# Optimization experiments

Measured on AMD Instinct MI355X. Metric: run time of the kernel, lower is better.

The kernel has to match this reference:

```python
import jax, jax.numpy as jnp
import numpy as np

B, T, EEG, GEO, TH, HID, OUT = 4096, 320, 64, 18, 32, 16, 4
THETA0, BETA, TAU_A, TAU_M, EPS = 0.5, 1.8, 0.36, 0.8, 1e-5


@jax.custom_vjp
def spike_fn(x):
    return jnp.where(x >= 0, 1.0, 0.0).astype(x.dtype)

def _spike_fwd(x):
    return spike_fn(x), x

def _spike_bwd(x, g):
    # SuperSpike-style surrogate gradient (original defvjp not shown in source)
    return (g / (10.0 * jnp.abs(x) + 1.0) ** 2,)

spike_fn.defvjp(_spike_fwd, _spike_bwd)


def setup_inputs() -> dict:
    key = jax.random.key(0)
    ks = jax.random.split(key, 20)
    rn = lambda k, s, sc=0.05: (jax.random.normal(k, s, jnp.float32) * sc)
    return {
        "x_eeg": jax.random.normal(ks[0], (B, T, EEG), jnp.float32),
        "x_geo": jax.random.normal(ks[1], (B, T, GEO), jnp.float32),
        "conv1_k": rn(ks[2], (5, EEG, TH)),   # (W, Cin, Cout)
        "conv1_b": jnp.zeros((TH,), jnp.float32),
        "bn1_scale": jnp.ones((TH,), jnp.float32),
        "bn1_bias": jnp.zeros((TH,), jnp.float32),
        "bn1_mean": rn(ks[3], (TH,)),
        "bn1_var": jnp.abs(rn(ks[4], (TH,))) + 1.0,
        "conv2_k": rn(ks[5], (3, TH, HID)),
        "conv2_b": jnp.zeros((HID,), jnp.float32),
        "bn2_scale": jnp.ones((HID,), jnp.float32),
        "bn2_bias": jnp.zeros((HID,), jnp.float32),
        "bn2_mean": rn(ks[6], (HID,)),
        "bn2_var": jnp.abs(rn(ks[7], (HID,))) + 1.0,
        "geo_W": rn(ks[8], (GEO, HID), 0.2),
        "geo_b": jnp.zeros((HID,), jnp.float32),
        "gamma": jnp.full((HID,), 0.5, jnp.float32),
        "fc1_W": rn(ks[9], (HID * 10, 64), 0.1),
        "fc1_b": jnp.zeros((64,), jnp.float32),
        "fc2_W": rn(ks[10], (64, OUT), 0.1),
        "fc2_b": jnp.zeros((OUT,), jnp.float32),
    }


def _conv1d(x, k, b, pad):
    # x: (B,T,C) NWC; k: (W,Cin,Cout) WIO
    return jax.lax.conv_general_dilated(
        x, k, window_strides=(1,), padding=[(pad, pad)],
        dimension_numbers=("NWC", "WIO", "NWC")) + b


def _bn(x, scale, bias, mean, var):
    return (x - mean) * jax.lax.rsqrt(var + EPS) * scale + bias


def reference(x_eeg, x_geo, conv1_k, conv1_b, bn1_scale, bn1_bias, bn1_mean,
              bn1_var, conv2_k, conv2_b, bn2_scale, bn2_bias, bn2_mean,
              bn2_var, geo_W, geo_b, gamma, fc1_W, fc1_b, fc2_W, fc2_b):
    x = jax.nn.relu(_bn(_conv1d(x_eeg, conv1_k, conv1_b, 2),
                        bn1_scale, bn1_bias, bn1_mean, bn1_var))
    eeg_encoded = jax.nn.relu(_bn(_conv1d(x, conv2_k, conv2_b, 1),
                                  bn2_scale, bn2_bias, bn2_mean, bn2_var))  # (B,T,HID)
    geo_mod = jax.nn.sigmoid(x_geo @ geo_W + geo_b)  # (B,T,HID)

    def scan_fn(carry, inputs):
        mem_alif, eta, mem_li, prev_spike = carry
        cur_eeg, cur_geo = inputs
        eta = TAU_A * eta + (1.0 - TAU_A) * prev_spike
        theta_t = THETA0 + BETA * eta - gamma * cur_geo
        mem_alif = TAU_M * mem_alif + cur_eeg
        spk = spike_fn(mem_alif - theta_t)
        mem_alif = mem_alif * (1.0 - spk)
        mem_li = 0.9 * mem_li + spk
        return (mem_alif, eta, mem_li, spk), mem_li

    z = jnp.zeros((B, HID), jnp.float32)
    _, mem_li_seq = jax.lax.scan(
        scan_fn, (z, z, z, z),
        (jnp.swapaxes(eeg_encoded, 0, 1), jnp.swapaxes(geo_mod, 0, 1)))
    mem_li_seq = jnp.swapaxes(jnp.swapaxes(mem_li_seq, 0, 1), 1, 2)  # (B,HID,T)

    windows = mem_li_seq.reshape(B, HID, 10, 32)
    dp_feat = (jnp.mean(windows[..., 16:], axis=-1) -
               jnp.mean(windows[..., :16], axis=-1)).reshape(B, -1)  # (B,160)
    out = jax.nn.relu(dp_feat @ fc1_W + fc1_b)
    return out @ fc2_W + fc2_b
```

## Files before the change

kernel.cpp:

```cpp
#include <hip/hip_runtime.h>

typedef _Float16 f16;
typedef __attribute__((ext_vector_type(8))) _Float16 f16x8;
typedef __attribute__((ext_vector_type(16))) float f32x16;

#define T_LEN 320

__device__ __forceinline__ void split2h(float v, unsigned short &h, unsigned short &l) {
    f16 hh = (f16)v;
    f16 ll = (f16)((v - (float)hh) * 4096.0f);
    h = __builtin_bit_cast(unsigned short, hh);
    l = __builtin_bit_cast(unsigned short, ll);
}

__global__ __launch_bounds__(256) void geo_prep_kernel(
    const float* __restrict__ k1, const float* __restrict__ c1b,
    const float* __restrict__ bn1s, const float* __restrict__ bn1b,
    const float* __restrict__ bn1m, const float* __restrict__ bn1v,
    const float* __restrict__ k2, const float* __restrict__ c2b,
    const float* __restrict__ bn2s, const float* __restrict__ bn2b,
    const float* __restrict__ bn2m, const float* __restrict__ bn2v,
    unsigned short* __restrict__ w1f, unsigned short* __restrict__ w2f,
    float* __restrict__ sb)
{
    const int tid = threadIdx.x;
    for (int e = tid; e < 20 * 64; e += 256) {
        const int ks = e >> 6, l = e & 63;
        const int lh = l >> 5, n = l & 31;
        for (int j = 0; j < 8; ++j) {
            const int kg = ks * 16 + lh * 8 + j;
            unsigned short h, lo; split2h(k1[kg * 32 + n], h, lo);
            w1f[((ks * 2 + 0) * 64 + l) * 8 + j] = h;
            w1f[((ks * 2 + 1) * 64 + l) * 8 + j] = lo;
        }
    }
    for (int e = tid; e < 6 * 64; e += 256) {
        const int ks = e >> 6, l = e & 63;
        const int lh = l >> 5, n = l & 31;
        for (int j = 0; j < 8; ++j) {
            const int kg = ks * 16 + lh * 8 + j;
            const float v = (n < 16) ? k2[kg * 16 + n] : 0.0f;
            unsigned short h, lo; split2h(v, h, lo);
            w2f[((ks * 2 + 0) * 64 + l) * 8 + j] = h;
            w2f[((ks * 2 + 1) * 64 + l) * 8 + j] = lo;
        }
    }
    if (tid < 32) {
        const float s1 = bn1s[tid] * (1.0f / sqrtf(bn1v[tid] + 1e-5f));
        sb[tid]      = s1;
        sb[32 + tid] = bn1b[tid] + (c1b[tid] - bn1m[tid]) * s1;
    }
    if (tid < 16) {
        const float s2 = bn2s[tid] * (1.0f / sqrtf(bn2v[tid] + 1e-5f));
        sb[64 + tid] = s2;
        sb[80 + tid] = bn2b[tid] + (c2b[tid] - bn2m[tid]) * s2;
    }
}

struct ConvSmem {
    unsigned short xh[70][64], xl[70][64];
    unsigned short c1h[66][40], c1l[66][40];
};

#define MFMA32(A, B, C) __builtin_amdgcn_mfma_f32_32x32x16_f16((A), (B), (C), 0, 0, 0)

__global__ __launch_bounds__(256, 4) void geo_alif_conv_kernel(
    const float* __restrict__ x_eeg,
    const unsigned short* __restrict__ w1f, const unsigned short* __restrict__ w2f,
    const float* __restrict__ sb, float* __restrict__ e_ws)
{
    __shared__ ConvSmem sm;
    const int tid = threadIdx.x, lane = tid & 63, wv = tid >> 6;
    const int l31 = lane & 31, lh = lane >> 5;
    const int row = blockIdx.x / 5, cc = blockIdx.x % 5;
    const int t0 = cc * 64;
    const float* xrow = x_eeg + (size_t)row * (T_LEN * 64);
    float* erow = e_ws + (size_t)row * (16 * T_LEN);

    {
        float4 v[5];
#pragma unroll
        for (int q = 0; q < 5; ++q) {
            const int fi = tid + q * 256;
            float4 tv = {0.f, 0.f, 0.f, 0.f};
            if (fi < 1120) {
                const int s = fi >> 4;
                const int tabs = t0 - 3 + s;
                if (tabs >= 0 && tabs < T_LEN)
                    tv = *reinterpret_cast<const float4*>(xrow + (size_t)tabs * 64 + (fi & 15) * 4);
            }
            v[q] = tv;
        }
#pragma unroll
        for (int q = 0; q < 5; ++q) {
            const int fi = tid + q * 256;
            if (fi < 1120) {
                const int s = fi >> 4, cq = fi & 15;
                unsigned short h0,l0,h1,l1,h2,l2,h3,l3;
                split2h(v[q].x, h0, l0); split2h(v[q].y, h1, l1);
                split2h(v[q].z, h2, l2); split2h(v[q].w, h3, l3);
                const int off = (((cq >> 1) ^ (s & 7)) * 8) + (cq & 1) * 4;
                ushort4 hv = {h0, h1, h2, h3}, lv = {l0, l1, l2, l3};
                *reinterpret_cast<ushort4*>(&sm.xh[s][off]) = hv;
                *reinterpret_cast<ushort4*>(&sm.xl[s][off]) = lv;
            }
        }
    }
    __syncthreads();

    if (wv < 3) {
        const int frag = wv;
        const float s1 = sb[l31], b1 = sb[32 + l31];
        const f16x8* w1v = reinterpret_cast<const f16x8*>(w1f);
        f32x16 am, cx;
#pragma unroll
        for (int q = 0; q < 16; ++q) { am[q] = 0.f; cx[q] = 0.f; }
        f16x8 pbh[4], pbl[4], pah[3], pal[3];
#pragma unroll
        for (int p = 0; p < 4; ++p) {
            pbh[p] = w1v[(p * 2 + 0) * 64 + lane];
            pbl[p] = w1v[(p * 2 + 1) * 64 + lane];
        }
#pragma unroll
        for (int p = 0; p < 3; ++p) {
            const int kb = p * 16 + lh * 8;
            int s = frag * 32 + l31 + (kb >> 6); if (s > 69) s = 69;
            const int off = ((((kb & 63) >> 3) ^ (s & 7)) * 8);
            pah[p] = *reinterpret_cast<const f16x8*>(&sm.xh[s][off]);
            pal[p] = *reinterpret_cast<const f16x8*>(&sm.xl[s][off]);
        }
#pragma unroll
        for (int ks = 0; ks < 20; ++ks) {
            const f16x8 ah = pah[ks % 3], al = pal[ks % 3];
            const f16x8 bh = pbh[ks % 4], bl = pbl[ks % 4];
            am = MFMA32(ah, bh, am);
            cx = MFMA32(ah, bl, cx);
            cx = MFMA32(al, bh, cx);
            if (ks < 17) {
                const int kb = (ks + 3) * 16 + lh * 8;
                int s = frag * 32 + l31 + (kb >> 6); if (s > 69) s = 69;
                const int off = ((((kb & 63) >> 3) ^ (s & 7)) * 8);
                pah[ks % 3] = *reinterpret_cast<const f16x8*>(&sm.xh[s][off]);
                pal[ks % 3] = *reinterpret_cast<const f16x8*>(&sm.xl[s][off]);
            }
            if (ks < 16) {
                pbh[ks % 4] = w1v[((ks + 4) * 2 + 0) * 64 + lane];
                pbl[ks % 4] = w1v[((ks + 4) * 2 + 1) * 64 + lane];
            }
        }
#pragma unroll
        for (int reg = 0; reg < 16; ++reg) {
            const int rl = frag * 32 + (reg & 3) + 8 * (reg >> 2) + 4 * lh;
            if (rl < 66) {
                const int tabs = t0 - 1 + rl;
                float v = am[reg] + cx[reg] * (1.0f / 4096.0f);
                v = (tabs >= 0 && tabs < T_LEN) ? fmaxf(v * s1 + b1, 0.0f) : 0.0f;
                unsigned short h_, lo_; split2h(v, h_, lo_);
                const int ui = (((l31 >> 3) ^ (rl & 3)) * 8) + (l31 & 7);
                sm.c1h[rl][ui] = h_;
                sm.c1l[rl][ui] = lo_;
            }
        }
    }
    __syncthreads();

    if (wv < 2) {
        const int mf = wv;
        const float s2 = (l31 < 16) ? sb[64 + l31] : 0.0f;
        const float b2 = (l31 < 16) ? sb[80 + l31] : 0.0f;
        const f16x8* w2v = reinterpret_cast<const f16x8*>(w2f);
        f16x8 w2hv[6], w2lv[6];
#pragma unroll
        for (int p = 0; p < 6; ++p) {
            w2hv[p] = w2v[(p * 2 + 0) * 64 + lane];
            w2lv[p] = w2v[(p * 2 + 1) * 64 + lane];
        }
        f32x16 am, cx;
#pragma unroll
        for (int q = 0; q < 16; ++q) { am[q] = 0.f; cx[q] = 0.f; }
#pragma unroll
        for (int ks = 0; ks < 6; ++ks) {
            const int kb = ks * 16 + lh * 8;
            const int sidx = mf * 32 + l31 + (kb >> 5);
            const int off = ((((kb & 31) >> 3) ^ (sidx & 3)) * 8);
            f16x8 ah = *reinterpret_cast<const f16x8*>(&sm.c1h[sidx][off]);
            f16x8 al = *reinterpret_cast<const f16x8*>(&sm.c1l[sidx][off]);
            am = MFMA32(ah, w2hv[ks], am);
            cx = MFMA32(ah, w2lv[ks], cx);
            cx = MFMA32(al, w2hv[ks], cx);
        }
        if (l31 < 16) {
#pragma unroll
            for (int reg = 0; reg < 16; ++reg) {
                const int t = t0 + mf * 32 + (reg & 3) + 8 * (reg >> 2) + 4 * lh;
                float v = am[reg] + cx[reg] * (1.0f / 4096.0f);
                v = fmaxf(v * s2 + b2, 0.0f);
                erow[(size_t)l31 * T_LEN + t] = v;
            }
        }
    }
}

__global__ __launch_bounds__(256) void geo_alif_scan_kernel(
    const float* __restrict__ e_ws, const float* __restrict__ x_geo,
    const float* __restrict__ geoW, const float* __restrict__ geob,
    const float* __restrict__ gam,
    const float* __restrict__ fc1W, const float* __restrict__ fc1b,
    const float* __restrict__ fc2W, const float* __restrict__ fc2b,
    float* __restrict__ out)
{
    __shared__ float xgf[16 * 292];
    __shared__ float dp[16 * 164];
    __shared__ float h1s[16 * 68];

    const int tid = threadIdx.x;
    const int r = tid >> 4, h = tid & 15;
    const int b0 = blockIdx.x * 16;
    const float* ep = e_ws + ((size_t)(b0 + r) * 16 + h) * T_LEN;
    const float gmv = gam[h];
    const float gb = geob[h];
    float gwr[18];
#pragma unroll
    for (int i = 0; i < 18; ++i) gwr[i] = geoW[i * 16 + h];

    for (int gi = tid; gi < 1152; gi += 256) {
        const int rg = gi / 72, q = gi - rg * 72;
        float4 tv = *reinterpret_cast<const float4*>(
            x_geo + ((size_t)(b0 + rg) * T_LEN) * 18 + q * 4);
        *reinterpret_cast<float4*>(&xgf[rg * 292 + q * 4]) = tv;
    }

    float mem = 0.f, eta = 0.f, li = 0.f, prev = 0.f, acc = 0.f;

    for (int c = 0; c < 20; ++c) {
        const float* ec = ep + c * 16;
        float4 ev0 = *reinterpret_cast<const float4*>(ec);
        float4 ev1 = *reinterpret_cast<const float4*>(ec + 4);
        float4 ev2 = *reinterpret_cast<const float4*>(ec + 8);
        float4 ev3 = *reinterpret_cast<const float4*>(ec + 12);

        __syncthreads();
        float thc[16];
#pragma unroll
        for (int tl = 0; tl < 16; ++tl) {
            float a = gb;
#pragma unroll
            for (int i = 0; i < 18; ++i)
                a = fmaf(xgf[r * 292 + tl * 18 + i], gwr[i], a);
            thc[tl] = 0.5f - gmv * (1.f / (1.f + expf(-a)));
        }
        __syncthreads();

        if (c < 19) {
            for (int gi = tid; gi < 1152; gi += 256) {
                const int rg = gi / 72, q = gi - rg * 72;
                float4 tv = *reinterpret_cast<const float4*>(
                    x_geo + ((size_t)(b0 + rg) * T_LEN + (c + 1) * 16) * 18 + q * 4);
                *reinterpret_cast<float4*>(&xgf[rg * 292 + q * 4]) = tv;
            }
        }

        float evs[16] = {ev0.x, ev0.y, ev0.z, ev0.w, ev1.x, ev1.y, ev1.z, ev1.w,
                         ev2.x, ev2.y, ev2.z, ev2.w, ev3.x, ev3.y, ev3.z, ev3.w};
#pragma unroll
        for (int u = 0; u < 16; ++u) {
            const int tt = c * 16 + u;
            eta = 0.36f * eta + 0.64f * prev;
            const float th = thc[u] + 1.8f * eta;
            mem = 0.8f * mem + evs[u];
            const bool sp = (mem >= th);
            const float spk = sp ? 1.f : 0.f;
            prev = spk;
            mem = sp ? 0.f : mem;
            li = 0.9f * li + spk;
            acc += ((tt & 31) < 16) ? -li : li;
            if ((tt & 31) == 31) {
                dp[r * 164 + h * 10 + (tt >> 5)] = acc * 0.0625f;
                acc = 0.f;
            }
        }
    }
    __syncthreads();

    {
        const int rr = tid >> 4, j0 = tid & 15;
        float a0 = fc1b[j0], a1 = fc1b[j0 + 16], a2 = fc1b[j0 + 32], a3 = fc1b[j0 + 48];
        for (int f = 0; f < 160; ++f) {
            const float d = dp[rr * 164 + f];
            a0 = fmaf(d, fc1W[f * 64 + j0],      a0);
            a1 = fmaf(d, fc1W[f * 64 + j0 + 16], a1);
            a2 = fmaf(d, fc1W[f * 64 + j0 + 32], a2);
            a3 = fmaf(d, fc1W[f * 64 + j0 + 48], a3);
        }
        h1s[rr * 68 + j0]      = fmaxf(a0, 0.f);
        h1s[rr * 68 + j0 + 16] = fmaxf(a1, 0.f);
        h1s[rr * 68 + j0 + 32] = fmaxf(a2, 0.f);
        h1s[rr * 68 + j0 + 48] = fmaxf(a3, 0.f);
    }
    __syncthreads();

    if (tid < 64) {
        const int rr = tid >> 2, o = tid & 3;
        float a = fc2b[o];
#pragma unroll
        for (int j = 0; j < 64; ++j) a = fmaf(h1s[rr * 68 + j], fc2W[j * 4 + o], a);
        out[((size_t)(b0 + rr)) * 4 + o] = a;
    }
}

extern "C" void kernel_launch(void* const* d_in, const int* in_sizes, int n_in,
                              void* d_out, int out_size, void* d_ws, size_t ws_size,
                              hipStream_t stream) {
    (void)in_sizes; (void)n_in; (void)out_size; (void)ws_size;
    const float* x_eeg = (const float*)d_in[0];
    const float* x_geo = (const float*)d_in[1];
    const float* k1    = (const float*)d_in[2];
    const float* c1b   = (const float*)d_in[3];
    const float* bn1s  = (const float*)d_in[4];
    const float* bn1b  = (const float*)d_in[5];
    const float* bn1m  = (const float*)d_in[6];
    const float* bn1v  = (const float*)d_in[7];
    const float* k2    = (const float*)d_in[8];
    const float* c2b   = (const float*)d_in[9];
    const float* bn2s  = (const float*)d_in[10];
    const float* bn2b  = (const float*)d_in[11];
    const float* bn2m  = (const float*)d_in[12];
    const float* bn2v  = (const float*)d_in[13];
    const float* geoW  = (const float*)d_in[14];
    const float* geob  = (const float*)d_in[15];
    const float* gam   = (const float*)d_in[16];
    const float* fc1W  = (const float*)d_in[17];
    const float* fc1b  = (const float*)d_in[18];
    const float* fc2W  = (const float*)d_in[19];
    const float* fc2b  = (const float*)d_in[20];

    char* wsb = (char*)d_ws;
    unsigned short* w1f = (unsigned short*)(wsb);
    unsigned short* w2f = (unsigned short*)(wsb + 40960);
    float* sb           = (float*)(wsb + 53248);
    float* e_ws         = (float*)(wsb + 65536);

    geo_prep_kernel<<<1, 256, 0, stream>>>(
        k1, c1b, bn1s, bn1b, bn1m, bn1v,
        k2, c2b, bn2s, bn2b, bn2m, bn2v, w1f, w2f, sb);

    geo_alif_conv_kernel<<<4096 * 5, 256, 0, stream>>>(x_eeg, w1f, w2f, sb, e_ws);

    geo_alif_scan_kernel<<<256, 256, 0, stream>>>(
        e_ws, x_geo, geoW, geob, gam, fc1W, fc1b, fc2W, fc2b, (float*)d_out);
}
```

Before: 311.3 us.

## Redistribute geo sigmoid work per timestep and vectorize conv output stores

In the scan kernel each thread now loads one (row, timestep) geo vector from global memory, computes all 16 hidden sigmoids and writes them to shared memory. Previously each thread computed its own hidden channel over 16 timesteps from a staged shared tile. The scan then reads the per-step sigmoid from shared memory. The conv kernel writes its output with float4 stores instead of scalar stores, and its occupancy hint rises from 4 to 5 blocks per CU. The aim is to spread the geo projection more evenly and cut store instruction count, at the cost of uncoalesced stride-18 global reads of x_geo and possible register pressure under the tighter launch bound.

```diff
diff --git a/kernel.cpp b/kernel.cpp
--- a/kernel.cpp
+++ b/kernel.cpp
@@ -64,7 +64,7 @@
 
 #define MFMA32(A, B, C) __builtin_amdgcn_mfma_f32_32x32x16_f16((A), (B), (C), 0, 0, 0)
 
-__global__ __launch_bounds__(256, 4) void geo_alif_conv_kernel(
+__global__ __launch_bounds__(256, 5) void geo_alif_conv_kernel(
     const float* __restrict__ x_eeg,
     const unsigned short* __restrict__ w1f, const unsigned short* __restrict__ w2f,
     const float* __restrict__ sb, float* __restrict__ e_ws)
@@ -191,11 +191,14 @@
         }
         if (l31 < 16) {
 #pragma unroll
-            for (int reg = 0; reg < 16; ++reg) {
-                const int t = t0 + mf * 32 + (reg & 3) + 8 * (reg >> 2) + 4 * lh;
-                float v = am[reg] + cx[reg] * (1.0f / 4096.0f);
-                v = fmaxf(v * s2 + b2, 0.0f);
-                erow[(size_t)l31 * T_LEN + t] = v;
+            for (int g = 0; g < 4; ++g) {
+                const int t = t0 + mf * 32 + 8 * g + 4 * lh;
+                float4 ov;
+                ov.x = fmaxf((am[g*4+0] + cx[g*4+0] * (1.0f/4096.0f)) * s2 + b2, 0.0f);
+                ov.y = fmaxf((am[g*4+1] + cx[g*4+1] * (1.0f/4096.0f)) * s2 + b2, 0.0f);
+                ov.z = fmaxf((am[g*4+2] + cx[g*4+2] * (1.0f/4096.0f)) * s2 + b2, 0.0f);
+                ov.w = fmaxf((am[g*4+3] + cx[g*4+3] * (1.0f/4096.0f)) * s2 + b2, 0.0f);
+                *reinterpret_cast<float4*>(erow + (size_t)l31 * T_LEN + t) = ov;
             }
         }
     }
@@ -209,26 +212,19 @@
     const float* __restrict__ fc2W, const float* __restrict__ fc2b,
     float* __restrict__ out)
 {
-    __shared__ float xgf[16 * 292];
-    __shared__ float dp[16 * 164];
-    __shared__ float h1s[16 * 68];
+    __shared__ float gW[18][16];
+    __shared__ float geo_s[16][16][16];
+    __shared__ float dp[16][160];
+    __shared__ float h1s[16][64];
 
     const int tid = threadIdx.x;
+    for (int i = tid; i < 288; i += 256) gW[i / 16][i & 15] = geoW[i];
+    __syncthreads();
+
     const int r = tid >> 4, h = tid & 15;
-    const int b0 = blockIdx.x * 16;
-    const float* ep = e_ws + ((size_t)(b0 + r) * 16 + h) * T_LEN;
+    const int b = blockIdx.x * 16 + r;
+    const float* ep = e_ws + ((size_t)b * 16 + h) * T_LEN;
     const float gmv = gam[h];
-    const float gb = geob[h];
-    float gwr[18];
-#pragma unroll
-    for (int i = 0; i < 18; ++i) gwr[i] = geoW[i * 16 + h];
-
-    for (int gi = tid; gi < 1152; gi += 256) {
-        const int rg = gi / 72, q = gi - rg * 72;
-        float4 tv = *reinterpret_cast<const float4*>(
-            x_geo + ((size_t)(b0 + rg) * T_LEN) * 18 + q * 4);
-        *reinterpret_cast<float4*>(&xgf[rg * 292 + q * 4]) = tv;
-    }
 
     float mem = 0.f, eta = 0.f, li = 0.f, prev = 0.f, acc = 0.f;
 
@@ -239,34 +235,31 @@
         float4 ev2 = *reinterpret_cast<const float4*>(ec + 8);
         float4 ev3 = *reinterpret_cast<const float4*>(ec + 12);
 
+        {
+            const int rg = tid >> 4, tl = tid & 15;
+            const int t = c * 16 + tl;
+            const float* xg = x_geo + ((size_t)(blockIdx.x * 16 + rg) * T_LEN + t) * 18;
+            float xv[18];
+#pragma unroll
+            for (int i = 0; i < 18; ++i) xv[i] = xg[i];
+#pragma unroll
+            for (int hh = 0; hh < 16; ++hh) {
+                float a = geob[hh];
+#pragma unroll
+                for (int i = 0; i < 18; ++i) a = fmaf(xv[i], gW[i][hh], a);
+                geo_s[rg][tl][hh] = 1.f / (1.f + expf(-a));
+            }
+        }
         __syncthreads();
-        float thc[16];
-#pragma unroll
-        for (int tl = 0; tl < 16; ++tl) {
-            float a = gb;
-#pragma unroll
-            for (int i = 0; i < 18; ++i)
-                a = fmaf(xgf[r * 292 + tl * 18 + i], gwr[i], a);
-            thc[tl] = 0.5f - gmv * (1.f / (1.f + expf(-a)));
-        }
-        __syncthreads();
-
-        if (c < 19) {
-            for (int gi = tid; gi < 1152; gi += 256) {
-                const int rg = gi / 72, q = gi - rg * 72;
-                float4 tv = *reinterpret_cast<const float4*>(
-                    x_geo + ((size_t)(b0 + rg) * T_LEN + (c + 1) * 16) * 18 + q * 4);
-                *reinterpret_cast<float4*>(&xgf[rg * 292 + q * 4]) = tv;
-            }
-        }
 
         float evs[16] = {ev0.x, ev0.y, ev0.z, ev0.w, ev1.x, ev1.y, ev1.z, ev1.w,
                          ev2.x, ev2.y, ev2.z, ev2.w, ev3.x, ev3.y, ev3.z, ev3.w};
 #pragma unroll
         for (int u = 0; u < 16; ++u) {
             const int tt = c * 16 + u;
+            const float g = geo_s[r][u][h];
             eta = 0.36f * eta + 0.64f * prev;
-            const float th = thc[u] + 1.8f * eta;
+            const float th = 0.5f + 1.8f * eta - gmv * g;
             mem = 0.8f * mem + evs[u];
             const bool sp = (mem >= th);
             const float spk = sp ? 1.f : 0.f;
@@ -275,27 +268,27 @@
             li = 0.9f * li + spk;
             acc += ((tt & 31) < 16) ? -li : li;
             if ((tt & 31) == 31) {
-                dp[r * 164 + h * 10 + (tt >> 5)] = acc * 0.0625f;
+                dp[r][h * 10 + (tt >> 5)] = acc * 0.0625f;
                 acc = 0.f;
             }
         }
-    }
-    __syncthreads();
+        __syncthreads();
+    }
 
     {
         const int rr = tid >> 4, j0 = tid & 15;
         float a0 = fc1b[j0], a1 = fc1b[j0 + 16], a2 = fc1b[j0 + 32], a3 = fc1b[j0 + 48];
         for (int f = 0; f < 160; ++f) {
-            const float d = dp[rr * 164 + f];
+            const float d = dp[rr][f];
             a0 = fmaf(d, fc1W[f * 64 + j0],      a0);
             a1 = fmaf(d, fc1W[f * 64 + j0 + 16], a1);
             a2 = fmaf(d, fc1W[f * 64 + j0 + 32], a2);
             a3 = fmaf(d, fc1W[f * 64 + j0 + 48], a3);
         }
-        h1s[rr * 68 + j0]      = fmaxf(a0, 0.f);
-        h1s[rr * 68 + j0 + 16] = fmaxf(a1, 0.f);
-        h1s[rr * 68 + j0 + 32] = fmaxf(a2, 0.f);
-        h1s[rr * 68 + j0 + 48] = fmaxf(a3, 0.f);
+        h1s[rr][j0]      = fmaxf(a0, 0.f);
+        h1s[rr][j0 + 16] = fmaxf(a1, 0.f);
+        h1s[rr][j0 + 32] = fmaxf(a2, 0.f);
+        h1s[rr][j0 + 48] = fmaxf(a3, 0.f);
     }
     __syncthreads();
 
@@ -303,8 +296,8 @@
         const int rr = tid >> 2, o = tid & 3;
         float a = fc2b[o];
 #pragma unroll
-        for (int j = 0; j < 64; ++j) a = fmaf(h1s[rr * 68 + j], fc2W[j * 4 + o], a);
-        out[((size_t)(b0 + rr)) * 4 + o] = a;
+        for (int j = 0; j < 64; ++j) a = fmaf(h1s[rr][j], fc2W[j * 4 + o], a);
+        out[((size_t)(blockIdx.x * 16 + rr)) * 4 + o] = a;
     }
 }
 
```

Result: faster. 281.0 us, median of 2 (-9.7%).
